# Kernel tuning notes

Measured on AMD Instinct MI355X. Metric: run time of the kernel, lower is better.

Reference implementation:

```python
import jax, jax.numpy as jnp
import numpy as np

H, C = 8, 32  # heads, out_channels
NEG_SLOPE = 0.2


def setup_inputs() -> dict:
    key = jax.random.key(0)
    k1, k2, k3, k4, k5 = jax.random.split(key, 5)
    N, IN, E, NNZ = 50000, 256, 10000, 320000
    X = jax.random.normal(k1, (N, IN), dtype=jnp.float32)
    # Linear(in, H*C, bias=False): weight [H*C, IN], scaled like kaiming-uniform-ish
    W = jax.random.normal(k2, (H * C, IN), dtype=jnp.float32) * (1.0 / np.sqrt(IN))
    # glorot init for att_e [1, H, C]
    stdv = np.sqrt(6.0 / (H + C))
    att_e = jax.random.uniform(k3, (1, H, C), dtype=jnp.float32, minval=-stdv, maxval=stdv)
    vertex = jax.random.randint(k4, (NNZ,), 0, N, dtype=jnp.int64)
    edges = jax.random.randint(k5, (NNZ,), 0, E, dtype=jnp.int64)
    return {"X": X, "W": W, "att_e": att_e, "vertex": vertex, "edges": edges, "num_edges": E}


def reference(X, W, att_e, vertex, edges, num_edges):
    N = X.shape[0]
    X0 = X @ W.T                                   # [N, H*C]
    Xh = X0.reshape(N, H, C)                       # [N, H, C]
    Xve = Xh[vertex]                               # [nnz, H, C] gather
    # scatter-mean over hyperedges (first_aggregate='mean')
    Xe_sum = jax.ops.segment_sum(Xve, edges, num_segments=num_edges)
    cnt = jax.ops.segment_sum(jnp.ones(vertex.shape, X.dtype), edges, num_segments=num_edges)
    Xe = Xe_sum / jnp.maximum(cnt, 1.0)[:, None, None]   # [E, H, C]
    alpha_e = (Xe * att_e).sum(-1)                 # [E, H]
    a_ev = alpha_e[edges]                          # [nnz, H]
    a = jax.nn.leaky_relu(a_ev, NEG_SLOPE)
    # segment softmax grouped by destination vertex
    amax = jax.ops.segment_max(a, vertex, num_segments=N)
    amax = jnp.where(jnp.isfinite(amax), amax, 0.0)
    ex = jnp.exp(a - amax[vertex])
    denom = jax.ops.segment_sum(ex, vertex, num_segments=N)
    alpha = ex / (denom[vertex] + 1e-16)           # [nnz, H]
    # attn-weighted scatter-sum back to vertices (dropout p=0.0 -> identity)
    Xev = Xe[edges] * alpha[:, :, None]            # [nnz, H, C]
    Xv = jax.ops.segment_sum(Xev, vertex, num_segments=N)  # [N, H, C]
    Xout = Xv.reshape(N, H * C)
    # use_norm: l2 row-normalize with detached norm
    norm = jax.lax.stop_gradient(jnp.linalg.norm(Xout, axis=1, keepdims=True))
    scale = jnp.where(norm > 0, 1.0 / norm, 0.0)
    return Xout * scale
```

## Files before the change

kernel.cpp:

```cpp
#include <hip/hip_runtime.h>
#include <cmath>

#define HC 256
#define H_ 8
#define C_ 32
#define E_CONST 10000
#define CAPE 160
#define CAPV 32
#define NEG_SLOPE 0.2f

typedef __attribute__((ext_vector_type(8))) short short8;
typedef __attribute__((ext_vector_type(4))) short short4v;
typedef __attribute__((ext_vector_type(4))) float f32x4;

static __device__ inline unsigned short f2bf(float f) {
    unsigned u = __float_as_uint(f);
    unsigned r = u + 0x7FFFu + ((u >> 16) & 1u);
    return (unsigned short)(r >> 16);
}
static __device__ inline float bf2f(unsigned short s) {
    return __uint_as_float(((unsigned)s) << 16);
}
static __device__ inline unsigned pk2bf(float lo, float hi) {
    return (unsigned)f2bf(lo) | ((unsigned)f2bf(hi) << 16);
}

#define GLD16(gp, lp) __builtin_amdgcn_global_load_lds( \
    (const __attribute__((address_space(1))) unsigned int*)(gp), \
    (__attribute__((address_space(3))) unsigned int*)(lp), 16, 0, 0)

__global__ __launch_bounds__(256) void k_pre(
        const float* __restrict__ X, const float* __restrict__ W,
        unsigned short* __restrict__ Xb, unsigned short* __restrict__ Wb,
        int nX, int nW) {
    int g = blockIdx.x * 256 + threadIdx.x;
    int nXg = nX >> 3;
    int nTg = (nX + nW) >> 3;
    if (g >= nTg) return;
    const float* src;
    unsigned short* dst;
    int base;
    if (g < nXg) { src = X; dst = Xb; base = g << 3; }
    else         { src = W; dst = Wb; base = (g - nXg) << 3; }
    float4 a = *(const float4*)(src + base);
    float4 b = *(const float4*)(src + base + 4);
    uint4 o;
    o.x = pk2bf(a.x, a.y);
    o.y = pk2bf(a.z, a.w);
    o.z = pk2bf(b.x, b.y);
    o.w = pk2bf(b.z, b.w);
    *(uint4*)(dst + base) = o;
}

__global__ __launch_bounds__(256) void k_gemm_fill(
        const unsigned short* __restrict__ Xb, const unsigned short* __restrict__ Wb,
        unsigned short* __restrict__ X0, int Nrows, int nbx, int fillBlocks,
        const int* __restrict__ vertex, const int* __restrict__ edges,
        int* cnt_e, int* cnt_v, int* bucket_e, int* bucket_v, int nnz) {
    if ((int)blockIdx.x < fillBlocks) {
        int i = blockIdx.x * 256 + threadIdx.x;
        if (i < nnz) {
            int v = vertex[i];
            int e = edges[i];
            int pe = atomicAdd(&cnt_e[e], 1);
            if (pe < CAPE) bucket_e[(size_t)e * CAPE + pe] = v;
            int pv = atomicAdd(&cnt_v[v], 1);
            if (pv < CAPV) bucket_v[(size_t)v * CAPV + pv] = e;
        }
        return;
    }
    __shared__ unsigned short As[128 * 64];
    __shared__ unsigned short Bs[128 * 64];
    const int bid  = blockIdx.x - fillBlocks;
    const int t    = threadIdx.x;
    const int lane = t & 63;
    const int wave = t >> 6;
    const int wr   = wave >> 1;
    const int wc   = wave & 1;
    const int bx   = bid % nbx;
    const int by   = bid / nbx;
    const int r0   = bx * 128;
    const int c0   = by * 128;
    const int ln15 = lane & 15;
    const int q8   = (lane >> 4) * 8;
    const int rw   = lane >> 3;
    const int cf   = (lane & 7) ^ rw;

    f32x4 acc[4][4];
    #pragma unroll
    for (int i = 0; i < 4; ++i)
        #pragma unroll
        for (int j = 0; j < 4; ++j) acc[i][j] = (f32x4){0.f, 0.f, 0.f, 0.f};

    for (int k0 = 0; k0 < 256; k0 += 64) {
        #pragma unroll
        for (int u = 0; u < 4; ++u) {
            int j   = u * 4 + wave;
            int row = j * 8 + rw;
            int gr  = r0 + row;
            if (gr < Nrows)
                GLD16(Xb + (size_t)gr * 256 + k0 + cf * 8, &As[j * 512]);
            GLD16(Wb + (size_t)(c0 + row) * 256 + k0 + cf * 8, &Bs[j * 512]);
        }
        __syncthreads();
        #pragma unroll
        for (int ks = 0; ks < 64; ks += 32) {
            int c = (ks + q8) >> 3;
            short8 af[4], bfr[4];
            #pragma unroll
            for (int mi = 0; mi < 4; ++mi) {
                int m   = wr * 64 + mi * 16 + ln15;
                int pos = c ^ (m & 7);
                af[mi] = *(const short8*)(&As[m * 64 + pos * 8]);
            }
            #pragma unroll
            for (int nj = 0; nj < 4; ++nj) {
                int n   = wc * 64 + nj * 16 + ln15;
                int pos = c ^ (n & 7);
                bfr[nj] = *(const short8*)(&Bs[n * 64 + pos * 8]);
            }
            #pragma unroll
            for (int mi = 0; mi < 4; ++mi)
                #pragma unroll
                for (int nj = 0; nj < 4; ++nj)
                    acc[mi][nj] = __builtin_amdgcn_mfma_f32_16x16x32_bf16(
                        af[mi], bfr[nj], acc[mi][nj], 0, 0, 0);
        }
        __syncthreads();
    }
    const int rowq = (lane >> 4) * 4;
    #pragma unroll
    for (int mi = 0; mi < 4; ++mi) {
        #pragma unroll
        for (int r = 0; r < 4; ++r) {
            int m = r0 + wr * 64 + mi * 16 + rowq + r;
            if (m < Nrows) {
                unsigned short* dst = X0 + (size_t)m * 256 + c0 + wc * 64 + ln15;
                #pragma unroll
                for (int nj = 0; nj < 4; ++nj) dst[nj * 16] = f2bf(acc[mi][nj][r]);
            }
        }
    }
}

__global__ __launch_bounds__(256) void k_edge_agg(const unsigned short* __restrict__ X0,
                                                  const float* __restrict__ att,
                                                  const int* __restrict__ cnt_e,
                                                  const int* __restrict__ bucket_e,
                                                  unsigned short* __restrict__ Xe,
                                                  float* __restrict__ alpha_e, int E) {
    int wave = (blockIdx.x * blockDim.x + threadIdx.x) >> 6;
    int l = threadIdx.x & 63;
    if (wave >= E) return;
    int e = wave;
    int m = cnt_e[e];
    if (m > CAPE) m = CAPE;
    const int* be = bucket_e + (size_t)e * CAPE;
    float4 accA = make_float4(0.f, 0.f, 0.f, 0.f);
    float4 accB = make_float4(0.f, 0.f, 0.f, 0.f);
    int j = 0;
    for (; j + 4 <= m; j += 4) {
        int v0 = be[j], v1 = be[j + 1], v2 = be[j + 2], v3 = be[j + 3];
        short4v x0 = *(const short4v*)(X0 + (size_t)v0 * 256 + 4 * l);
        short4v x1 = *(const short4v*)(X0 + (size_t)v1 * 256 + 4 * l);
        short4v x2 = *(const short4v*)(X0 + (size_t)v2 * 256 + 4 * l);
        short4v x3 = *(const short4v*)(X0 + (size_t)v3 * 256 + 4 * l);
        accA.x += bf2f(x0[0]) + bf2f(x1[0]); accB.x += bf2f(x2[0]) + bf2f(x3[0]);
        accA.y += bf2f(x0[1]) + bf2f(x1[1]); accB.y += bf2f(x2[1]) + bf2f(x3[1]);
        accA.z += bf2f(x0[2]) + bf2f(x1[2]); accB.z += bf2f(x2[2]) + bf2f(x3[2]);
        accA.w += bf2f(x0[3]) + bf2f(x1[3]); accB.w += bf2f(x2[3]) + bf2f(x3[3]);
    }
    for (; j < m; ++j) {
        int v0 = be[j];
        short4v x0 = *(const short4v*)(X0 + (size_t)v0 * 256 + 4 * l);
        accA.x += bf2f(x0[0]); accA.y += bf2f(x0[1]);
        accA.z += bf2f(x0[2]); accA.w += bf2f(x0[3]);
    }
    float4 acc = make_float4(accA.x + accB.x, accA.y + accB.y,
                             accA.z + accB.z, accA.w + accB.w);
    float inv = 1.0f / (float)(m > 1 ? m : 1);
    acc.x *= inv; acc.y *= inv; acc.z *= inv; acc.w *= inv;
    short4v xs = {(short)f2bf(acc.x), (short)f2bf(acc.y),
                  (short)f2bf(acc.z), (short)f2bf(acc.w)};
    *(short4v*)(Xe + (size_t)e * 256 + 4 * l) = xs;
    int h  = l >> 3;
    int c8 = (l & 7) << 2;
    float4 av = *(const float4*)(att + h * 32 + c8);
    float s = acc.x * av.x + acc.y * av.y + acc.z * av.z + acc.w * av.w;
    s += __shfl_xor(s, 1, 8);
    s += __shfl_xor(s, 2, 8);
    s += __shfl_xor(s, 4, 8);
    if ((l & 7) == 0) {
        float a = s > 0.f ? s : NEG_SLOPE * s;
        alpha_e[e * H_ + h] = a;
    }
}

__global__ __launch_bounds__(256) void k_vertex_agg(const unsigned short* __restrict__ Xe,
                                                    const float* __restrict__ alpha_e,
                                                    const int* __restrict__ cnt_v,
                                                    const int* __restrict__ bucket_v,
                                                    float* __restrict__ out, int N) {
    int wid = (blockIdx.x * blockDim.x + threadIdx.x) >> 6;
    int l = threadIdx.x & 63;
    if (wid >= N) return;
    int v = wid;
    int m = cnt_v[v];
    if (m > CAPV) m = CAPV;
    const int* bv = bucket_v + (size_t)v * CAPV;
    int jl = l >> 3, hp = l & 7;
    float aa[4];
    #pragma unroll
    for (int b = 0; b < 4; ++b) {
        int jj = b * 8 + jl;
        aa[b] = (jj < m) ? alpha_e[bv[jj] * H_ + hp] : -INFINITY;
    }
    float amax = fmaxf(fmaxf(aa[0], aa[1]), fmaxf(aa[2], aa[3]));
    amax = fmaxf(amax, __shfl_xor(amax, 8, 64));
    amax = fmaxf(amax, __shfl_xor(amax, 16, 64));
    amax = fmaxf(amax, __shfl_xor(amax, 32, 64));
    float ex[4];
    float dsum = 0.f;
    #pragma unroll
    for (int b = 0; b < 4; ++b) {
        ex[b] = __expf(aa[b] - amax);
        dsum += ex[b];
    }
    dsum += __shfl_xor(dsum, 8, 64);
    dsum += __shfl_xor(dsum, 16, 64);
    dsum += __shfl_xor(dsum, 32, 64);
    float rden = 1.0f / (dsum + 1e-16f);
    int h2 = l >> 3;
    float rden2 = __shfl(rden, h2, 64);
    float4 acc0 = make_float4(0.f, 0.f, 0.f, 0.f);
    float4 acc1 = make_float4(0.f, 0.f, 0.f, 0.f);
    #pragma unroll
    for (int b = 0; b < 4; ++b) {
        int lo = b * 8;
        if (lo >= m) break;
        int hi = m < lo + 8 ? m : lo + 8;
        int j = lo;
        for (; j + 2 <= hi; j += 2) {
            int e0 = bv[j], e1 = bv[j + 1];
            float p0 = __shfl(ex[b], (((j) & 7) << 3) | h2, 64) * rden2;
            float p1 = __shfl(ex[b], (((j + 1) & 7) << 3) | h2, 64) * rden2;
            short4v x0 = *(const short4v*)(Xe + (size_t)e0 * 256 + 4 * l);
            short4v x1 = *(const short4v*)(Xe + (size_t)e1 * 256 + 4 * l);
            acc0.x += p0 * bf2f(x0[0]); acc1.x += p1 * bf2f(x1[0]);
            acc0.y += p0 * bf2f(x0[1]); acc1.y += p1 * bf2f(x1[1]);
            acc0.z += p0 * bf2f(x0[2]); acc1.z += p1 * bf2f(x1[2]);
            acc0.w += p0 * bf2f(x0[3]); acc1.w += p1 * bf2f(x1[3]);
        }
        if (j < hi) {
            int e0 = bv[j];
            float p0 = __shfl(ex[b], (((j) & 7) << 3) | h2, 64) * rden2;
            short4v x0 = *(const short4v*)(Xe + (size_t)e0 * 256 + 4 * l);
            acc0.x += p0 * bf2f(x0[0]); acc0.y += p0 * bf2f(x0[1]);
            acc0.z += p0 * bf2f(x0[2]); acc0.w += p0 * bf2f(x0[3]);
        }
    }
    float4 acc = make_float4(acc0.x + acc1.x, acc0.y + acc1.y,
                             acc0.z + acc1.z, acc0.w + acc1.w);
    float ss = acc.x * acc.x + acc.y * acc.y + acc.z * acc.z + acc.w * acc.w;
    #pragma unroll
    for (int off = 1; off < 64; off <<= 1) ss += __shfl_xor(ss, off, 64);
    float scale = ss > 0.f ? 1.0f / sqrtf(ss) : 0.f;
    float4 o = make_float4(acc.x * scale, acc.y * scale, acc.z * scale, acc.w * scale);
    *(float4*)(out + (size_t)v * 256 + 4 * l) = o;
}

extern "C" void kernel_launch(void* const* d_in, const int* in_sizes, int n_in,
                              void* d_out, int out_size, void* d_ws, size_t ws_size,
                              hipStream_t stream) {
    const float* X      = (const float*)d_in[0];
    const float* W      = (const float*)d_in[1];
    const float* att    = (const float*)d_in[2];
    const int*   vertex = (const int*)d_in[3];
    const int*   edges  = (const int*)d_in[4];
    const int NNZ = in_sizes[3];
    const int N   = in_sizes[0] / 256;
    const int nX  = in_sizes[0];
    const int nW  = in_sizes[1];
    const int E   = E_CONST;

    char* ws = (char*)d_ws;
    unsigned short* Xb = (unsigned short*)ws; ws += (size_t)nX * 2;
    unsigned short* Wb = (unsigned short*)ws; ws += (size_t)nW * 2;
    unsigned short* X0 = (unsigned short*)ws; ws += (size_t)N * HC * 2;
    unsigned short* Xe = (unsigned short*)ws; ws += (size_t)E * HC * 2;
    float* alpha_e  = (float*)ws; ws += (size_t)E * H_ * 4;
    int*   cnt_e    = (int*)ws;   ws += (size_t)E * 4;
    int*   cnt_v    = (int*)ws;   ws += (size_t)N * 4;
    int*   bucket_e = (int*)ws;   ws += (size_t)E * CAPE * 4;
    int*   bucket_v = (int*)ws;

    hipMemsetAsync(cnt_e, 0, (size_t)(E + N) * 4, stream);

    const int cvtBlocks = (((nX + nW) >> 3) + 255) / 256;
    k_pre<<<cvtBlocks, 256, 0, stream>>>(X, W, Xb, Wb, nX, nW);

    const int nbx = (N + 127) / 128;
    const int fillBlocks = (NNZ + 255) / 256;
    k_gemm_fill<<<fillBlocks + nbx * 2, 256, 0, stream>>>(
        Xb, Wb, X0, N, nbx, fillBlocks, vertex, edges,
        cnt_e, cnt_v, bucket_e, bucket_v, NNZ);

    k_edge_agg<<<(E * 64 + 255) / 256, 256, 0, stream>>>(X0, att, cnt_e, bucket_e,
                                                         Xe, alpha_e, E);
    k_vertex_agg<<<(N * 64 + 255) / 256, 256, 0, stream>>>(Xe, alpha_e, cnt_v, bucket_v,
                                                           (float*)d_out, N);
}
```

Baseline: 220.5 us.

## Aggregate raw inputs per hyperedge before projection and fold attention into weights

Because the projection is linear, the hyperedge mean is now taken over the bf16 inputs and the GEMM runs on the E edge means instead of all N vertex rows. This removes most of the GEMM work and the write-back of the large per-vertex projected matrix. The attention vector is pre-folded into W as w_att, so alpha_e comes straight from the mean. Bucket entries shrink to 16-bit indices and the counters are padded to reduce atomic contention. Risks: an extra bf16 rounding of the mean before the GEMM, 16-bit indices that only hold while N stays below 65536, and a larger memset for the padded counters.

```diff
diff --git a/kernel.cpp b/kernel.cpp
--- a/kernel.cpp
+++ b/kernel.cpp
@@ -7,6 +7,7 @@
 #define E_CONST 10000
 #define CAPE 160
 #define CAPV 32
+#define CSTRIDE 16
 #define NEG_SLOPE 0.2f
 
 typedef __attribute__((ext_vector_type(8))) short short8;
@@ -31,9 +32,42 @@
 
 __global__ __launch_bounds__(256) void k_pre(
         const float* __restrict__ X, const float* __restrict__ W,
+        const float* __restrict__ att,
         unsigned short* __restrict__ Xb, unsigned short* __restrict__ Wb,
-        int nX, int nW) {
-    int g = blockIdx.x * 256 + threadIdx.x;
+        float* __restrict__ w_att, int nX, int nW, int fillB,
+        const int* __restrict__ vertex, const int* __restrict__ edges,
+        int* cnt_e, int* cnt_v,
+        unsigned short* bucket_e, unsigned short* bucket_v, int nnz) {
+    const int bid = blockIdx.x;
+    const int t   = threadIdx.x;
+    if (bid == 0) {
+        float acc[H_] = {};
+        for (int c = 0; c < C_; ++c) {
+            #pragma unroll
+            for (int h = 0; h < H_; ++h)
+                acc[h] += W[(size_t)(h * C_ + c) * 256 + t] * att[h * C_ + c];
+        }
+        #pragma unroll
+        for (int h = 0; h < H_; ++h) w_att[h * 256 + t] = acc[h];
+        return;
+    }
+    if (bid <= fillB) {
+        int base = (bid - 1) * 1024;
+        #pragma unroll
+        for (int u = 0; u < 4; ++u) {
+            int i = base + u * 256 + t;
+            if (i < nnz) {
+                int v = vertex[i];
+                int e = edges[i];
+                int pe = atomicAdd(&cnt_e[e * CSTRIDE], 1);
+                if (pe < CAPE) bucket_e[(size_t)e * CAPE + pe] = (unsigned short)v;
+                int pv = atomicAdd(&cnt_v[v * CSTRIDE], 1);
+                if (pv < CAPV) bucket_v[(size_t)v * CAPV + pv] = (unsigned short)e;
+            }
+        }
+        return;
+    }
+    int g = (bid - 1 - fillB) * 256 + t;
     int nXg = nX >> 3;
     int nTg = (nX + nW) >> 3;
     if (g >= nTg) return;
@@ -52,33 +86,79 @@
     *(uint4*)(dst + base) = o;
 }
 
-__global__ __launch_bounds__(256) void k_gemm_fill(
-        const unsigned short* __restrict__ Xb, const unsigned short* __restrict__ Wb,
-        unsigned short* __restrict__ X0, int Nrows, int nbx, int fillBlocks,
-        const int* __restrict__ vertex, const int* __restrict__ edges,
-        int* cnt_e, int* cnt_v, int* bucket_e, int* bucket_v, int nnz) {
-    if ((int)blockIdx.x < fillBlocks) {
-        int i = blockIdx.x * 256 + threadIdx.x;
-        if (i < nnz) {
-            int v = vertex[i];
-            int e = edges[i];
-            int pe = atomicAdd(&cnt_e[e], 1);
-            if (pe < CAPE) bucket_e[(size_t)e * CAPE + pe] = v;
-            int pv = atomicAdd(&cnt_v[v], 1);
-            if (pv < CAPV) bucket_v[(size_t)v * CAPV + pv] = e;
-        }
-        return;
-    }
+__global__ __launch_bounds__(256) void k_edge_mean(
+        const unsigned short* __restrict__ Xb,
+        const float* __restrict__ w_att,
+        const int* __restrict__ cnt_e,
+        const unsigned short* __restrict__ bucket_e,
+        unsigned short* __restrict__ Xm,
+        float* __restrict__ alpha_e, int E) {
+    int wid = (blockIdx.x * blockDim.x + threadIdx.x) >> 6;
+    int l = threadIdx.x & 63;
+    if (wid >= E) return;
+    int e = wid;
+    int m = cnt_e[e * CSTRIDE];
+    if (m > CAPE) m = CAPE;
+    const unsigned short* be = bucket_e + (size_t)e * CAPE;
+    float4 accA = make_float4(0.f, 0.f, 0.f, 0.f);
+    float4 accB = make_float4(0.f, 0.f, 0.f, 0.f);
+    int j = 0;
+    for (; j + 4 <= m; j += 4) {
+        int v0 = be[j], v1 = be[j + 1], v2 = be[j + 2], v3 = be[j + 3];
+        short4v x0 = *(const short4v*)(Xb + (size_t)v0 * 256 + 4 * l);
+        short4v x1 = *(const short4v*)(Xb + (size_t)v1 * 256 + 4 * l);
+        short4v x2 = *(const short4v*)(Xb + (size_t)v2 * 256 + 4 * l);
+        short4v x3 = *(const short4v*)(Xb + (size_t)v3 * 256 + 4 * l);
+        accA.x += bf2f(x0[0]) + bf2f(x1[0]); accB.x += bf2f(x2[0]) + bf2f(x3[0]);
+        accA.y += bf2f(x0[1]) + bf2f(x1[1]); accB.y += bf2f(x2[1]) + bf2f(x3[1]);
+        accA.z += bf2f(x0[2]) + bf2f(x1[2]); accB.z += bf2f(x2[2]) + bf2f(x3[2]);
+        accA.w += bf2f(x0[3]) + bf2f(x1[3]); accB.w += bf2f(x2[3]) + bf2f(x3[3]);
+    }
+    for (; j < m; ++j) {
+        int v0 = be[j];
+        short4v x0 = *(const short4v*)(Xb + (size_t)v0 * 256 + 4 * l);
+        accA.x += bf2f(x0[0]); accA.y += bf2f(x0[1]);
+        accA.z += bf2f(x0[2]); accA.w += bf2f(x0[3]);
+    }
+    float4 mean = make_float4(accA.x + accB.x, accA.y + accB.y,
+                              accA.z + accB.z, accA.w + accB.w);
+    float inv = 1.0f / (float)(m > 1 ? m : 1);
+    mean.x *= inv; mean.y *= inv; mean.z *= inv; mean.w *= inv;
+    short4v xs = {(short)f2bf(mean.x), (short)f2bf(mean.y),
+                  (short)f2bf(mean.z), (short)f2bf(mean.w)};
+    *(short4v*)(Xm + (size_t)e * 256 + 4 * l) = xs;
+    float s[H_];
+    #pragma unroll
+    for (int h = 0; h < H_; ++h) {
+        float4 wv = *(const float4*)(w_att + h * 256 + 4 * l);
+        s[h] = mean.x * wv.x + mean.y * wv.y + mean.z * wv.z + mean.w * wv.w;
+    }
+    #pragma unroll
+    for (int off = 1; off < 64; off <<= 1)
+        #pragma unroll
+        for (int h = 0; h < H_; ++h) s[h] += __shfl_xor(s[h], off, 64);
+    if (l == 0) {
+        #pragma unroll
+        for (int h = 0; h < H_; ++h) {
+            float a = s[h] > 0.f ? s[h] : NEG_SLOPE * s[h];
+            alpha_e[e * H_ + h] = a;
+        }
+    }
+}
+
+__global__ __launch_bounds__(256) void k_gemm(const unsigned short* __restrict__ Ain,
+                                              const unsigned short* __restrict__ Bin,
+                                              unsigned short* __restrict__ Cout,
+                                              int Nrows, int nbx) {
     __shared__ unsigned short As[128 * 64];
     __shared__ unsigned short Bs[128 * 64];
-    const int bid  = blockIdx.x - fillBlocks;
     const int t    = threadIdx.x;
     const int lane = t & 63;
     const int wave = t >> 6;
     const int wr   = wave >> 1;
     const int wc   = wave & 1;
-    const int bx   = bid % nbx;
-    const int by   = bid / nbx;
+    const int bx   = blockIdx.x % nbx;
+    const int by   = blockIdx.x / nbx;
     const int r0   = bx * 128;
     const int c0   = by * 128;
     const int ln15 = lane & 15;
@@ -99,8 +179,8 @@
             int row = j * 8 + rw;
             int gr  = r0 + row;
             if (gr < Nrows)
-                GLD16(Xb + (size_t)gr * 256 + k0 + cf * 8, &As[j * 512]);
-            GLD16(Wb + (size_t)(c0 + row) * 256 + k0 + cf * 8, &Bs[j * 512]);
+                GLD16(Ain + (size_t)gr * 256 + k0 + cf * 8, &As[j * 512]);
+            GLD16(Bin + (size_t)(c0 + row) * 256 + k0 + cf * 8, &Bs[j * 512]);
         }
         __syncthreads();
         #pragma unroll
@@ -109,15 +189,15 @@
             short8 af[4], bfr[4];
             #pragma unroll
             for (int mi = 0; mi < 4; ++mi) {
-                int m   = wr * 64 + mi * 16 + ln15;
-                int pos = c ^ (m & 7);
-                af[mi] = *(const short8*)(&As[m * 64 + pos * 8]);
+                int mm  = wr * 64 + mi * 16 + ln15;
+                int pos = c ^ (mm & 7);
+                af[mi] = *(const short8*)(&As[mm * 64 + pos * 8]);
             }
             #pragma unroll
             for (int nj = 0; nj < 4; ++nj) {
-                int n   = wc * 64 + nj * 16 + ln15;
-                int pos = c ^ (n & 7);
-                bfr[nj] = *(const short8*)(&Bs[n * 64 + pos * 8]);
+                int nn  = wc * 64 + nj * 16 + ln15;
+                int pos = c ^ (nn & 7);
+                bfr[nj] = *(const short8*)(&Bs[nn * 64 + pos * 8]);
             }
             #pragma unroll
             for (int mi = 0; mi < 4; ++mi)
@@ -133,9 +213,9 @@
     for (int mi = 0; mi < 4; ++mi) {
         #pragma unroll
         for (int r = 0; r < 4; ++r) {
-            int m = r0 + wr * 64 + mi * 16 + rowq + r;
-            if (m < Nrows) {
-                unsigned short* dst = X0 + (size_t)m * 256 + c0 + wc * 64 + ln15;
+            int mm = r0 + wr * 64 + mi * 16 + rowq + r;
+            if (mm < Nrows) {
+                unsigned short* dst = Cout + (size_t)mm * 256 + c0 + wc * 64 + ln15;
                 #pragma unroll
                 for (int nj = 0; nj < 4; ++nj) dst[nj * 16] = f2bf(acc[mi][nj][r]);
             }
@@ -143,77 +223,25 @@
     }
 }
 
-__global__ __launch_bounds__(256) void k_edge_agg(const unsigned short* __restrict__ X0,
-                                                  const float* __restrict__ att,
-                                                  const int* __restrict__ cnt_e,
-                                                  const int* __restrict__ bucket_e,
-                                                  unsigned short* __restrict__ Xe,
-                                                  float* __restrict__ alpha_e, int E) {
-    int wave = (blockIdx.x * blockDim.x + threadIdx.x) >> 6;
-    int l = threadIdx.x & 63;
-    if (wave >= E) return;
-    int e = wave;
-    int m = cnt_e[e];
-    if (m > CAPE) m = CAPE;
-    const int* be = bucket_e + (size_t)e * CAPE;
-    float4 accA = make_float4(0.f, 0.f, 0.f, 0.f);
-    float4 accB = make_float4(0.f, 0.f, 0.f, 0.f);
-    int j = 0;
-    for (; j + 4 <= m; j += 4) {
-        int v0 = be[j], v1 = be[j + 1], v2 = be[j + 2], v3 = be[j + 3];
-        short4v x0 = *(const short4v*)(X0 + (size_t)v0 * 256 + 4 * l);
-        short4v x1 = *(const short4v*)(X0 + (size_t)v1 * 256 + 4 * l);
-        short4v x2 = *(const short4v*)(X0 + (size_t)v2 * 256 + 4 * l);
-        short4v x3 = *(const short4v*)(X0 + (size_t)v3 * 256 + 4 * l);
-        accA.x += bf2f(x0[0]) + bf2f(x1[0]); accB.x += bf2f(x2[0]) + bf2f(x3[0]);
-        accA.y += bf2f(x0[1]) + bf2f(x1[1]); accB.y += bf2f(x2[1]) + bf2f(x3[1]);
-        accA.z += bf2f(x0[2]) + bf2f(x1[2]); accB.z += bf2f(x2[2]) + bf2f(x3[2]);
-        accA.w += bf2f(x0[3]) + bf2f(x1[3]); accB.w += bf2f(x2[3]) + bf2f(x3[3]);
-    }
-    for (; j < m; ++j) {
-        int v0 = be[j];
-        short4v x0 = *(const short4v*)(X0 + (size_t)v0 * 256 + 4 * l);
-        accA.x += bf2f(x0[0]); accA.y += bf2f(x0[1]);
-        accA.z += bf2f(x0[2]); accA.w += bf2f(x0[3]);
-    }
-    float4 acc = make_float4(accA.x + accB.x, accA.y + accB.y,
-                             accA.z + accB.z, accA.w + accB.w);
-    float inv = 1.0f / (float)(m > 1 ? m : 1);
-    acc.x *= inv; acc.y *= inv; acc.z *= inv; acc.w *= inv;
-    short4v xs = {(short)f2bf(acc.x), (short)f2bf(acc.y),
-                  (short)f2bf(acc.z), (short)f2bf(acc.w)};
-    *(short4v*)(Xe + (size_t)e * 256 + 4 * l) = xs;
-    int h  = l >> 3;
-    int c8 = (l & 7) << 2;
-    float4 av = *(const float4*)(att + h * 32 + c8);
-    float s = acc.x * av.x + acc.y * av.y + acc.z * av.z + acc.w * av.w;
-    s += __shfl_xor(s, 1, 8);
-    s += __shfl_xor(s, 2, 8);
-    s += __shfl_xor(s, 4, 8);
-    if ((l & 7) == 0) {
-        float a = s > 0.f ? s : NEG_SLOPE * s;
-        alpha_e[e * H_ + h] = a;
-    }
-}
-
-__global__ __launch_bounds__(256) void k_vertex_agg(const unsigned short* __restrict__ Xe,
-                                                    const float* __restrict__ alpha_e,
-                                                    const int* __restrict__ cnt_v,
-                                                    const int* __restrict__ bucket_v,
-                                                    float* __restrict__ out, int N) {
+__global__ __launch_bounds__(256) void k_vertex_agg(
+        const unsigned short* __restrict__ Xe,
+        const float* __restrict__ alpha_e,
+        const int* __restrict__ cnt_v,
+        const unsigned short* __restrict__ bucket_v,
+        float* __restrict__ out, int N) {
     int wid = (blockIdx.x * blockDim.x + threadIdx.x) >> 6;
     int l = threadIdx.x & 63;
     if (wid >= N) return;
     int v = wid;
-    int m = cnt_v[v];
+    int m = cnt_v[v * CSTRIDE];
     if (m > CAPV) m = CAPV;
-    const int* bv = bucket_v + (size_t)v * CAPV;
+    const unsigned short* bv = bucket_v + (size_t)v * CAPV;
     int jl = l >> 3, hp = l & 7;
     float aa[4];
     #pragma unroll
     for (int b = 0; b < 4; ++b) {
         int jj = b * 8 + jl;
-        aa[b] = (jj < m) ? alpha_e[bv[jj] * H_ + hp] : -INFINITY;
+        aa[b] = (jj < m) ? alpha_e[(int)bv[jj] * H_ + hp] : -INFINITY;
     }
     float amax = fmaxf(fmaxf(aa[0], aa[1]), fmaxf(aa[2], aa[3]));
     amax = fmaxf(amax, __shfl_xor(amax, 8, 64));
@@ -242,7 +270,7 @@
         int j = lo;
         for (; j + 2 <= hi; j += 2) {
             int e0 = bv[j], e1 = bv[j + 1];
-            float p0 = __shfl(ex[b], (((j) & 7) << 3) | h2, 64) * rden2;
+            float p0 = __shfl(ex[b], ((j & 7) << 3) | h2, 64) * rden2;
             float p1 = __shfl(ex[b], (((j + 1) & 7) << 3) | h2, 64) * rden2;
             short4v x0 = *(const short4v*)(Xe + (size_t)e0 * 256 + 4 * l);
             short4v x1 = *(const short4v*)(Xe + (size_t)e1 * 256 + 4 * l);
@@ -253,7 +281,7 @@
         }
         if (j < hi) {
             int e0 = bv[j];
-            float p0 = __shfl(ex[b], (((j) & 7) << 3) | h2, 64) * rden2;
+            float p0 = __shfl(ex[b], ((j & 7) << 3) | h2, 64) * rden2;
             short4v x0 = *(const short4v*)(Xe + (size_t)e0 * 256 + 4 * l);
             acc0.x += p0 * bf2f(x0[0]); acc0.y += p0 * bf2f(x0[1]);
             acc0.z += p0 * bf2f(x0[2]); acc0.w += p0 * bf2f(x0[3]);
@@ -286,27 +314,29 @@
     char* ws = (char*)d_ws;
     unsigned short* Xb = (unsigned short*)ws; ws += (size_t)nX * 2;
     unsigned short* Wb = (unsigned short*)ws; ws += (size_t)nW * 2;
-    unsigned short* X0 = (unsigned short*)ws; ws += (size_t)N * HC * 2;
+    unsigned short* Xm = (unsigned short*)ws; ws += (size_t)E * HC * 2;
     unsigned short* Xe = (unsigned short*)ws; ws += (size_t)E * HC * 2;
+    float* w_att    = (float*)ws; ws += (size_t)H_ * 256 * 4;
     float* alpha_e  = (float*)ws; ws += (size_t)E * H_ * 4;
-    int*   cnt_e    = (int*)ws;   ws += (size_t)E * 4;
-    int*   cnt_v    = (int*)ws;   ws += (size_t)N * 4;
-    int*   bucket_e = (int*)ws;   ws += (size_t)E * CAPE * 4;
-    int*   bucket_v = (int*)ws;
-
-    hipMemsetAsync(cnt_e, 0, (size_t)(E + N) * 4, stream);
-
-    const int cvtBlocks = (((nX + nW) >> 3) + 255) / 256;
-    k_pre<<<cvtBlocks, 256, 0, stream>>>(X, W, Xb, Wb, nX, nW);
-
-    const int nbx = (N + 127) / 128;
-    const int fillBlocks = (NNZ + 255) / 256;
-    k_gemm_fill<<<fillBlocks + nbx * 2, 256, 0, stream>>>(
-        Xb, Wb, X0, N, nbx, fillBlocks, vertex, edges,
-        cnt_e, cnt_v, bucket_e, bucket_v, NNZ);
-
-    k_edge_agg<<<(E * 64 + 255) / 256, 256, 0, stream>>>(X0, att, cnt_e, bucket_e,
-                                                         Xe, alpha_e, E);
-    k_vertex_agg<<<(N * 64 + 255) / 256, 256, 0, stream>>>(Xe, alpha_e, cnt_v, bucket_v,
-                                                           (float*)d_out, N);
-}
+    int*   cnt_e    = (int*)ws;   ws += (size_t)E * CSTRIDE * 4;
+    int*   cnt_v    = (int*)ws;   ws += (size_t)N * CSTRIDE * 4;
+    unsigned short* bucket_e = (unsigned short*)ws; ws += (size_t)E * CAPE * 2;
+    unsigned short* bucket_v = (unsigned short*)ws;
+
+    hipMemsetAsync(cnt_e, 0, (size_t)(E + N) * CSTRIDE * 4, stream);
+
+    const int fillB = (NNZ + 1023) / 1024;
+    const int cvtB  = (((nX + nW) >> 3) + 255) / 256;
+    k_pre<<<1 + fillB + cvtB, 256, 0, stream>>>(
+        X, W, att, Xb, Wb, w_att, nX, nW, fillB,
+        vertex, edges, cnt_e, cnt_v, bucket_e, bucket_v, NNZ);
+
+    k_edge_mean<<<(E * 64 + 255) / 256, 256, 0, stream>>>(
+        Xb, w_att, cnt_e, bucket_e, Xm, alpha_e, E);
+
+    const int nbx = (E + 127) / 128;
+    k_gemm<<<nbx * 2, 256, 0, stream>>>(Xm, Wb, Xe, E, nbx);
+
+    k_vertex_agg<<<(N * 64 + 255) / 256, 256, 0, stream>>>(
+        Xe, alpha_e, cnt_v, bucket_v, (float*)d_out, N);
+}
```

After: 206.2 us. -6.5%, faster.
